# Kernel optimization log

Measured on AMD Instinct MI355X. Metric: run time of the kernel, lower is better.

## Reference

```python
import jax, jax.numpy as jnp
import numpy as np

NDIV = (10, 10)
OUT_CHANNEL = 100


def setup_inputs() -> dict:
    key = jax.random.key(0)
    k1, k2 = jax.random.split(key)
    x1 = jax.random.normal(k1, (8, 64, 128, 128), dtype=jnp.float32)
    x2 = jax.random.normal(k2, (8, 64, 60, 60), dtype=jnp.float32)
    return {"x1": x1, "x2": x2}


def reference(x1, x2):
    B, C, H, W = x1.shape
    h, w = x2.shape[-2], x2.shape[-1]
    nd0, nd1 = NDIV
    hh, ww = h // nd0, w // nd1  # patch size (6, 6)
    P = nd0 * nd1                # 100 patches per sample

    # channel-wise L2 normalization (dim=1)
    x1n = x1 / jnp.linalg.norm(x1, axis=1, keepdims=True)
    x2n = x2 / jnp.linalg.norm(x2, axis=1, keepdims=True)

    # extract nd0*nd1 patches per sample as conv filters: [B*P, C, hh, ww]
    patches = x2n.reshape(B, C, nd0, hh, nd1, ww)
    patches = patches.transpose(0, 2, 4, 1, 3, 5).reshape(B * P, C, hh, ww)

    # grouped cross-correlation (torch F.conv2d = correlation, no kernel flip)
    lhs = x1n.reshape(1, B * C, H, W)
    mm = jax.lax.conv_general_dilated(
        lhs, patches,
        window_strides=(1, 1),
        padding=((hh // 2, hh // 2), (ww // 2, ww // 2)),
        feature_group_count=B,
        dimension_numbers=("NCHW", "OIHW", "NCHW"),
    ) / (hh * ww)  # [1, B*P, H+1, W+1] for even hh,ww

    # bilinear resize to (H, W)  (torch align_corners=False == half-pixel)
    mm = jax.image.resize(mm, (1, B * P, H, W), method="bilinear")

    # [B, P, H, W] -> topk over patch dim, then mean
    mm = mm.reshape(B, P, H, W)
    topv = jax.lax.top_k(jnp.moveaxis(mm, 1, -1), OUT_CHANNEL)[0]  # [B,H,W,k]
    out = jnp.mean(topv, axis=-1)[:, None]  # [B,1,H,W]
    return out
```

## Files before the change

kernel.cpp:

```cpp
#include <hip/hip_runtime.h>
#include <cstddef>
#include <cstdint>

#define BB   8
#define CC   64
#define H1   128
#define W1   128
#define HW1  (H1*W1)
#define HS   60
#define WS   60
#define HO   129
#define WO   129
#define NPIX (HS*WS)

#define UPL  (BB*HW1)

typedef _Float16 f16;
typedef __attribute__((ext_vector_type(2))) _Float16 h2;

#if __has_builtin(__builtin_amdgcn_fdot2)
#define FDOT2(a, b, c) __builtin_amdgcn_fdot2((a), (b), (c), false)
#else
#define FDOT2(a, b, c) ((c) + (float)(a)[0] * (float)(b)[0] + (float)(a)[1] * (float)(b)[1])
#endif

static __device__ __forceinline__ h2 pack_h2(float lo, float hi) {
#if __has_builtin(__builtin_amdgcn_cvt_pkrtz)
    return __builtin_bit_cast(h2, __builtin_amdgcn_cvt_pkrtz(lo, hi));
#else
    h2 r; r[0] = (f16)lo; r[1] = (f16)hi; return r;
#endif
}

__global__ __launch_bounds__(256) void k_inv2(const float* __restrict__ x2,
                                              float* __restrict__ inv2) {
    __shared__ float red[256];
    int tid = threadIdx.x;
    int pix = blockIdx.x * 64 + (tid & 63);
    int q   = tid >> 6;

    int b  = pix / NPIX;
    int hw = pix - b * NPIX;
    const float* p = x2 + (size_t)b * CC * NPIX + (size_t)(q * 16) * NPIX + hw;

    float s = 0.f;
#pragma unroll
    for (int cc = 0; cc < 16; cc += 8) {
        float v0 = p[(cc+0)*NPIX], v1 = p[(cc+1)*NPIX];
        float v2 = p[(cc+2)*NPIX], v3 = p[(cc+3)*NPIX];
        float v4 = p[(cc+4)*NPIX], v5 = p[(cc+5)*NPIX];
        float v6 = p[(cc+6)*NPIX], v7 = p[(cc+7)*NPIX];
        s += v0*v0 + v1*v1 + v2*v2 + v3*v3 + v4*v4 + v5*v5 + v6*v6 + v7*v7;
    }
    red[tid] = s;
    __syncthreads();
    if (tid < 64) {
        float t = red[tid] + red[tid + 64] + red[tid + 128] + red[tid + 192];
        inv2[blockIdx.x * 64 + tid] = 1.0f / sqrtf(t);
    }
}

__global__ __launch_bounds__(256) void k_fold(const float* __restrict__ x2,
                                              const float* __restrict__ inv2,
                                              f16* __restrict__ Sh) {
    __shared__ __align__(16) float pl[NPIX];
    __shared__ float red[256];
    int tid = threadIdx.x;
    int bc  = blockIdx.x;
    int b   = bc >> 6;
    int c   = bc & 63;

    const float* px = x2 + (size_t)bc * NPIX;
    const float* pn = inv2 + (size_t)b * NPIX;

    const float4* px4 = (const float4*)px;
    const float4* pn4 = (const float4*)pn;
    float4* pl4 = (float4*)pl;
    for (int i = tid; i < NPIX / 4; i += 256) {
        float4 a = px4[i];
        float4 w = pn4[i];
        pl4[i] = make_float4(a.x * w.x, a.y * w.y, a.z * w.z, a.w * w.w);
    }
    __syncthreads();

    float s = 0.f;
    if (tid < 252) {
        int bin = tid / 7, k = tid - bin * 7;
        int r = bin / 6, c6 = bin - r * 6;
        for (int e = k; e < 100; e += 7) {
            int i = e / 10, j = e - i * 10;
            s += pl[(r + 6 * i) * WS + (c6 + 6 * j)];
        }
    }
    red[tid] = s;
    __syncthreads();

    if (tid < 36) {
        const float* q = red + tid * 7;
        float bin = q[0] + q[1] + q[2] + q[3] + q[4] + q[5] + q[6];
        Sh[(((size_t)b * 32 + (c >> 1)) * 36 + tid) * 2 + (c & 1)] = (f16)bin;
    }
}

__global__ __launch_bounds__(256) void k_gemm(const float* __restrict__ x1,
                                              const f16* __restrict__ Sh,
                                              f16* __restrict__ U) {
    int blk = (blockIdx.x & 7) * 64 + (blockIdx.x >> 3);
    int b = blk >> 6;
    int p = (blk & 63) * 256 + threadIdx.x;

    const float* xp = x1 + (size_t)b * CC * HW1 + p;
    const uint32_t* Sw = (const uint32_t*)Sh + (size_t)b * (32 * 36);

    float acc[36];
#pragma unroll
    for (int t = 0; t < 36; ++t) acc[t] = 0.f;
    float s2 = 0.f;

#pragma unroll 2
    for (int cc = 0; cc < CC; cc += 8) {
        float v[8];
#pragma unroll
        for (int j = 0; j < 8; ++j)
            v[j] = __builtin_nontemporal_load(&xp[(size_t)(cc + j) * HW1]);
        h2 a[4];
#pragma unroll
        for (int q = 0; q < 4; ++q) {
            a[q] = pack_h2(v[2*q], v[2*q+1]);
            s2 += v[2*q] * v[2*q] + v[2*q+1] * v[2*q+1];
        }
#pragma unroll
        for (int q = 0; q < 4; ++q) {
            const uint32_t* sq = Sw + (size_t)(cc / 2 + q) * 36;
#pragma unroll
            for (int t = 0; t < 36; ++t) {
                h2 sv = __builtin_bit_cast(h2, sq[t]);
                acc[t] = FDOT2(a[q], sv, acc[t]);
            }
        }
    }

    float inv = (1.0f / 3600.0f) / sqrtf(s2);
    f16* up = U + (size_t)b * HW1 + p;
#pragma unroll
    for (int t = 0; t < 36; ++t) up[(size_t)t * UPL] = (f16)(acc[t] * inv);
}

__global__ __launch_bounds__(256) void k_out(const f16* __restrict__ U,
                                             float* __restrict__ out) {
    __shared__ float m[20 * 21];
    int blk  = (blockIdx.x & 7) * 64 + (blockIdx.x >> 3);
    int b    = blk >> 6;
    int tile = blk & 63;
    int oy0 = (tile >> 3) * 16, ox0 = (tile & 7) * 16;
    int ry0 = oy0 - 1, rx0 = ox0 - 1;
    int tid = threadIdx.x;

    const f16* Ub = U + (size_t)b * HW1;

    bool interior = (ry0 >= 3) && (ry0 + 19 <= 125) && (rx0 >= 3) && (rx0 + 19 <= 125);

    if (interior) {
        const f16* base = Ub + (size_t)(ry0 - 3) * W1 + (rx0 - 3);
        for (int i = tid; i < 400; i += 256) {
            int ly = i / 20, lx = i - ly * 20;
            const f16* pp = base + (size_t)ly * W1 + lx;
            float s = 0.f;
#pragma unroll
            for (int t = 0; t < 36; ++t) {
                int dy = t / 6, dx = t - dy * 6;
                s += (float)pp[(size_t)t * UPL + dy * W1 + dx];
            }
            m[ly * 21 + lx] = s;
        }
    } else {
        for (int i = tid; i < 400; i += 256) {
            int ly = i / 20, lx = i - ly * 20;
            int jy = min(max(ry0 + ly, 0), 128);
            int jx = min(max(rx0 + lx, 0), 128);
            float s = 0.f;
#pragma unroll
            for (int t = 0; t < 36; ++t) {
                int dy = t / 6, dx = t - dy * 6;
                int py = jy - 3 + dy, px = jx - 3 + dx;
                if ((unsigned)py < 128u && (unsigned)px < 128u)
                    s += (float)Ub[(size_t)t * UPL + py * W1 + px];
            }
            m[ly * 21 + lx] = s;
        }
    }
    __syncthreads();

    const float inv_scale = 129.0f / 128.0f;
    const float ksc       = 128.0f / 129.0f;

    int oy = oy0 + (tid >> 4);
    int ox = ox0 + (tid & 15);

    float sy = (oy + 0.5f) * inv_scale - 0.5f;
    float sx = (ox + 0.5f) * inv_scale - 0.5f;
    int fy = (int)floorf(sy);
    int fx = (int)floorf(sx);

    float wy[4], wx[4];
    float sumy = 0.f, sumx = 0.f;
#pragma unroll
    for (int k = 0; k < 4; ++k) {
        int jy = fy - 1 + k;
        float w = 0.f;
        if (jy >= 0 && jy < HO) w = fmaxf(0.f, 1.0f - fabsf(sy - (float)jy) * ksc);
        wy[k] = w; sumy += w;
        int jx = fx - 1 + k;
        float w2 = 0.f;
        if (jx >= 0 && jx < WO) w2 = fmaxf(0.f, 1.0f - fabsf(sx - (float)jx) * ksc);
        wx[k] = w2; sumx += w2;
    }

    float r = 0.f;
#pragma unroll
    for (int ky = 0; ky < 4; ++ky) {
        if (wy[ky] == 0.f) continue;
        int ly = fy - 1 + ky - ry0;
        float rowv = 0.f;
#pragma unroll
        for (int kx = 0; kx < 4; ++kx) {
            if (wx[kx] == 0.f) continue;
            int lx = fx - 1 + kx - rx0;
            rowv += wx[kx] * m[ly * 21 + lx];
        }
        r += wy[ky] * rowv;
    }

    out[(size_t)b * HW1 + oy * W1 + ox] = r / (sumy * sumx);
}

extern "C" void kernel_launch(void* const* d_in, const int* in_sizes, int n_in,
                              void* d_out, int out_size, void* d_ws, size_t ws_size,
                              hipStream_t stream) {
    const float* x1 = (const float*)d_in[0];
    const float* x2 = (const float*)d_in[1];
    float* out = (float*)d_out;

    float* ws   = (float*)d_ws;
    float* inv2 = ws;
    f16*   Sh   = (f16*)(inv2 + BB * NPIX);
    f16*   U    = (f16*)((char*)Sh + (size_t)BB * CC * 36 * sizeof(f16));

    k_inv2<<<BB * NPIX / 64, 256, 0, stream>>>(x2, inv2);
    k_fold<<<BB * CC, 256, 0, stream>>>(x2, inv2, Sh);
    k_gemm<<<BB * 64, 256, 0, stream>>>(x1, Sh, U);
    k_out <<<BB * 64, 256, 0, stream>>>(U, out);
}
```

Baseline: 114.5 us.

## Fuse four stage kernels into one cooperative kernel with grid syncs

Merges the inv-norm, fold, GEMM and resize/output kernels into a single persistent cooperative kernel, with grid-wide barriers between stages. This removes three kernel launch boundaries and their drain/ramp gaps. In exchange it adds grid.sync overhead and a launch-bounds occupancy hint that may constrain registers for the 36-accumulator GEMM stage. It also relies on all 512 blocks being co-resident for the cooperative launch to succeed.

```diff
diff --git a/kernel.cpp b/kernel.cpp
--- a/kernel.cpp
+++ b/kernel.cpp
@@ -1,6 +1,9 @@
 #include <hip/hip_runtime.h>
+#include <hip/hip_cooperative_groups.h>
 #include <cstddef>
 #include <cstdint>
+
+namespace cg = cooperative_groups;
 
 #define BB   8
 #define CC   64
@@ -32,206 +35,208 @@
 #endif
 }
 
-__global__ __launch_bounds__(256) void k_inv2(const float* __restrict__ x2,
-                                              float* __restrict__ inv2) {
-    __shared__ float red[256];
+__global__ __launch_bounds__(256, 2) void k_all(const float* __restrict__ x1,
+                                                const float* __restrict__ x2,
+                                                float* __restrict__ inv2,
+                                                f16* __restrict__ Sh,
+                                                f16* __restrict__ U,
+                                                float* __restrict__ out) {
+    cg::grid_group grid = cg::this_grid();
+    __shared__ __align__(16) float smem[NPIX + 256];
+
     int tid = threadIdx.x;
-    int pix = blockIdx.x * 64 + (tid & 63);
-    int q   = tid >> 6;
-
-    int b  = pix / NPIX;
-    int hw = pix - b * NPIX;
-    const float* p = x2 + (size_t)b * CC * NPIX + (size_t)(q * 16) * NPIX + hw;
-
-    float s = 0.f;
-#pragma unroll
-    for (int cc = 0; cc < 16; cc += 8) {
-        float v0 = p[(cc+0)*NPIX], v1 = p[(cc+1)*NPIX];
-        float v2 = p[(cc+2)*NPIX], v3 = p[(cc+3)*NPIX];
-        float v4 = p[(cc+4)*NPIX], v5 = p[(cc+5)*NPIX];
-        float v6 = p[(cc+6)*NPIX], v7 = p[(cc+7)*NPIX];
-        s += v0*v0 + v1*v1 + v2*v2 + v3*v3 + v4*v4 + v5*v5 + v6*v6 + v7*v7;
-    }
-    red[tid] = s;
-    __syncthreads();
-    if (tid < 64) {
-        float t = red[tid] + red[tid + 64] + red[tid + 128] + red[tid + 192];
-        inv2[blockIdx.x * 64 + tid] = 1.0f / sqrtf(t);
-    }
-}
-
-__global__ __launch_bounds__(256) void k_fold(const float* __restrict__ x2,
-                                              const float* __restrict__ inv2,
-                                              f16* __restrict__ Sh) {
-    __shared__ __align__(16) float pl[NPIX];
-    __shared__ float red[256];
-    int tid = threadIdx.x;
-    int bc  = blockIdx.x;
-    int b   = bc >> 6;
-    int c   = bc & 63;
-
-    const float* px = x2 + (size_t)bc * NPIX;
-    const float* pn = inv2 + (size_t)b * NPIX;
-
-    const float4* px4 = (const float4*)px;
-    const float4* pn4 = (const float4*)pn;
-    float4* pl4 = (float4*)pl;
-    for (int i = tid; i < NPIX / 4; i += 256) {
-        float4 a = px4[i];
-        float4 w = pn4[i];
-        pl4[i] = make_float4(a.x * w.x, a.y * w.y, a.z * w.z, a.w * w.w);
-    }
-    __syncthreads();
-
-    float s = 0.f;
-    if (tid < 252) {
-        int bin = tid / 7, k = tid - bin * 7;
-        int r = bin / 6, c6 = bin - r * 6;
-        for (int e = k; e < 100; e += 7) {
-            int i = e / 10, j = e - i * 10;
-            s += pl[(r + 6 * i) * WS + (c6 + 6 * j)];
-        }
-    }
-    red[tid] = s;
-    __syncthreads();
-
-    if (tid < 36) {
-        const float* q = red + tid * 7;
-        float bin = q[0] + q[1] + q[2] + q[3] + q[4] + q[5] + q[6];
-        Sh[(((size_t)b * 32 + (c >> 1)) * 36 + tid) * 2 + (c & 1)] = (f16)bin;
-    }
-}
-
-__global__ __launch_bounds__(256) void k_gemm(const float* __restrict__ x1,
-                                              const f16* __restrict__ Sh,
-                                              f16* __restrict__ U) {
-    int blk = (blockIdx.x & 7) * 64 + (blockIdx.x >> 3);
-    int b = blk >> 6;
-    int p = (blk & 63) * 256 + threadIdx.x;
-
-    const float* xp = x1 + (size_t)b * CC * HW1 + p;
-    const uint32_t* Sw = (const uint32_t*)Sh + (size_t)b * (32 * 36);
-
-    float acc[36];
-#pragma unroll
-    for (int t = 0; t < 36; ++t) acc[t] = 0.f;
-    float s2 = 0.f;
+    int blk0 = blockIdx.x;
+
+    if (blk0 < 450) {
+        float* red = smem;
+        int pix = blk0 * 64 + (tid & 63);
+        int q   = tid >> 6;
+        int b  = pix / NPIX;
+        int hw = pix - b * NPIX;
+        const float* p = x2 + (size_t)b * CC * NPIX + (size_t)(q * 16) * NPIX + hw;
+        float s = 0.f;
+#pragma unroll
+        for (int cc = 0; cc < 16; cc += 8) {
+            float v0 = p[(cc+0)*NPIX], v1 = p[(cc+1)*NPIX];
+            float v2 = p[(cc+2)*NPIX], v3 = p[(cc+3)*NPIX];
+            float v4 = p[(cc+4)*NPIX], v5 = p[(cc+5)*NPIX];
+            float v6 = p[(cc+6)*NPIX], v7 = p[(cc+7)*NPIX];
+            s += v0*v0 + v1*v1 + v2*v2 + v3*v3 + v4*v4 + v5*v5 + v6*v6 + v7*v7;
+        }
+        red[tid] = s;
+        __syncthreads();
+        if (tid < 64) {
+            float t = red[tid] + red[tid + 64] + red[tid + 128] + red[tid + 192];
+            inv2[blk0 * 64 + tid] = 1.0f / sqrtf(t);
+        }
+    }
+    grid.sync();
+
+    {
+        float* pl  = smem;
+        float* red = smem + NPIX;
+        int bc = blk0;
+        int b  = bc >> 6;
+        int c  = bc & 63;
+
+        const float4* px4 = (const float4*)(x2 + (size_t)bc * NPIX);
+        const float4* pn4 = (const float4*)(inv2 + (size_t)b * NPIX);
+        float4* pl4 = (float4*)pl;
+        for (int i = tid; i < NPIX / 4; i += 256) {
+            float4 a = px4[i];
+            float4 w = pn4[i];
+            pl4[i] = make_float4(a.x * w.x, a.y * w.y, a.z * w.z, a.w * w.w);
+        }
+        __syncthreads();
+
+        float s = 0.f;
+        if (tid < 252) {
+            int bin = tid / 7, k = tid - bin * 7;
+            int r = bin / 6, c6 = bin - r * 6;
+            for (int e = k; e < 100; e += 7) {
+                int i = e / 10, j = e - i * 10;
+                s += pl[(r + 6 * i) * WS + (c6 + 6 * j)];
+            }
+        }
+        red[tid] = s;
+        __syncthreads();
+
+        if (tid < 36) {
+            const float* q = red + tid * 7;
+            float bin = q[0] + q[1] + q[2] + q[3] + q[4] + q[5] + q[6];
+            Sh[(((size_t)b * 32 + (c >> 1)) * 36 + tid) * 2 + (c & 1)] = (f16)bin;
+        }
+    }
+    grid.sync();
+
+    {
+        int blk = (blk0 & 7) * 64 + (blk0 >> 3);
+        int b = blk >> 6;
+        int p = (blk & 63) * 256 + tid;
+
+        const float* xp = x1 + (size_t)b * CC * HW1 + p;
+        const uint32_t* Sw = (const uint32_t*)Sh + (size_t)b * (32 * 36);
+
+        float acc[36];
+#pragma unroll
+        for (int t = 0; t < 36; ++t) acc[t] = 0.f;
+        float s2 = 0.f;
 
 #pragma unroll 2
-    for (int cc = 0; cc < CC; cc += 8) {
-        float v[8];
-#pragma unroll
-        for (int j = 0; j < 8; ++j)
-            v[j] = __builtin_nontemporal_load(&xp[(size_t)(cc + j) * HW1]);
-        h2 a[4];
-#pragma unroll
-        for (int q = 0; q < 4; ++q) {
-            a[q] = pack_h2(v[2*q], v[2*q+1]);
-            s2 += v[2*q] * v[2*q] + v[2*q+1] * v[2*q+1];
-        }
-#pragma unroll
-        for (int q = 0; q < 4; ++q) {
-            const uint32_t* sq = Sw + (size_t)(cc / 2 + q) * 36;
-#pragma unroll
-            for (int t = 0; t < 36; ++t) {
-                h2 sv = __builtin_bit_cast(h2, sq[t]);
-                acc[t] = FDOT2(a[q], sv, acc[t]);
-            }
-        }
-    }
-
-    float inv = (1.0f / 3600.0f) / sqrtf(s2);
-    f16* up = U + (size_t)b * HW1 + p;
-#pragma unroll
-    for (int t = 0; t < 36; ++t) up[(size_t)t * UPL] = (f16)(acc[t] * inv);
-}
-
-__global__ __launch_bounds__(256) void k_out(const f16* __restrict__ U,
-                                             float* __restrict__ out) {
-    __shared__ float m[20 * 21];
-    int blk  = (blockIdx.x & 7) * 64 + (blockIdx.x >> 3);
-    int b    = blk >> 6;
-    int tile = blk & 63;
-    int oy0 = (tile >> 3) * 16, ox0 = (tile & 7) * 16;
-    int ry0 = oy0 - 1, rx0 = ox0 - 1;
-    int tid = threadIdx.x;
-
-    const f16* Ub = U + (size_t)b * HW1;
-
-    bool interior = (ry0 >= 3) && (ry0 + 19 <= 125) && (rx0 >= 3) && (rx0 + 19 <= 125);
-
-    if (interior) {
-        const f16* base = Ub + (size_t)(ry0 - 3) * W1 + (rx0 - 3);
-        for (int i = tid; i < 400; i += 256) {
-            int ly = i / 20, lx = i - ly * 20;
-            const f16* pp = base + (size_t)ly * W1 + lx;
-            float s = 0.f;
-#pragma unroll
-            for (int t = 0; t < 36; ++t) {
-                int dy = t / 6, dx = t - dy * 6;
-                s += (float)pp[(size_t)t * UPL + dy * W1 + dx];
-            }
-            m[ly * 21 + lx] = s;
-        }
-    } else {
-        for (int i = tid; i < 400; i += 256) {
-            int ly = i / 20, lx = i - ly * 20;
-            int jy = min(max(ry0 + ly, 0), 128);
-            int jx = min(max(rx0 + lx, 0), 128);
-            float s = 0.f;
-#pragma unroll
-            for (int t = 0; t < 36; ++t) {
-                int dy = t / 6, dx = t - dy * 6;
-                int py = jy - 3 + dy, px = jx - 3 + dx;
-                if ((unsigned)py < 128u && (unsigned)px < 128u)
-                    s += (float)Ub[(size_t)t * UPL + py * W1 + px];
-            }
-            m[ly * 21 + lx] = s;
-        }
-    }
-    __syncthreads();
-
-    const float inv_scale = 129.0f / 128.0f;
-    const float ksc       = 128.0f / 129.0f;
-
-    int oy = oy0 + (tid >> 4);
-    int ox = ox0 + (tid & 15);
-
-    float sy = (oy + 0.5f) * inv_scale - 0.5f;
-    float sx = (ox + 0.5f) * inv_scale - 0.5f;
-    int fy = (int)floorf(sy);
-    int fx = (int)floorf(sx);
-
-    float wy[4], wx[4];
-    float sumy = 0.f, sumx = 0.f;
-#pragma unroll
-    for (int k = 0; k < 4; ++k) {
-        int jy = fy - 1 + k;
-        float w = 0.f;
-        if (jy >= 0 && jy < HO) w = fmaxf(0.f, 1.0f - fabsf(sy - (float)jy) * ksc);
-        wy[k] = w; sumy += w;
-        int jx = fx - 1 + k;
-        float w2 = 0.f;
-        if (jx >= 0 && jx < WO) w2 = fmaxf(0.f, 1.0f - fabsf(sx - (float)jx) * ksc);
-        wx[k] = w2; sumx += w2;
-    }
-
-    float r = 0.f;
-#pragma unroll
-    for (int ky = 0; ky < 4; ++ky) {
-        if (wy[ky] == 0.f) continue;
-        int ly = fy - 1 + ky - ry0;
-        float rowv = 0.f;
-#pragma unroll
-        for (int kx = 0; kx < 4; ++kx) {
-            if (wx[kx] == 0.f) continue;
-            int lx = fx - 1 + kx - rx0;
-            rowv += wx[kx] * m[ly * 21 + lx];
-        }
-        r += wy[ky] * rowv;
-    }
-
-    out[(size_t)b * HW1 + oy * W1 + ox] = r / (sumy * sumx);
+        for (int cc = 0; cc < CC; cc += 8) {
+            float v[8];
+#pragma unroll
+            for (int j = 0; j < 8; ++j)
+                v[j] = __builtin_nontemporal_load(&xp[(size_t)(cc + j) * HW1]);
+            h2 a[4];
+#pragma unroll
+            for (int q = 0; q < 4; ++q) {
+                a[q] = pack_h2(v[2*q], v[2*q+1]);
+                s2 += v[2*q] * v[2*q] + v[2*q+1] * v[2*q+1];
+            }
+#pragma unroll
+            for (int q = 0; q < 4; ++q) {
+                const uint32_t* sq = Sw + (size_t)(cc / 2 + q) * 36;
+#pragma unroll
+                for (int t = 0; t < 36; ++t) {
+                    h2 sv = __builtin_bit_cast(h2, sq[t]);
+                    acc[t] = FDOT2(a[q], sv, acc[t]);
+                }
+            }
+        }
+
+        float inv = (1.0f / 3600.0f) / sqrtf(s2);
+        f16* up = U + (size_t)b * HW1 + p;
+#pragma unroll
+        for (int t = 0; t < 36; ++t) up[(size_t)t * UPL] = (f16)(acc[t] * inv);
+    }
+    grid.sync();
+
+    {
+        float* m = smem;
+        int blk  = (blk0 & 7) * 64 + (blk0 >> 3);
+        int b    = blk >> 6;
+        int tile = blk & 63;
+        int oy0 = (tile >> 3) * 16, ox0 = (tile & 7) * 16;
+        int ry0 = oy0 - 1, rx0 = ox0 - 1;
+
+        const f16* Ub = U + (size_t)b * HW1;
+
+        bool interior = (ry0 >= 3) && (ry0 + 19 <= 125) && (rx0 >= 3) && (rx0 + 19 <= 125);
+
+        if (interior) {
+            const f16* base = Ub + (size_t)(ry0 - 3) * W1 + (rx0 - 3);
+            for (int i = tid; i < 400; i += 256) {
+                int ly = i / 20, lx = i - ly * 20;
+                const f16* pp = base + (size_t)ly * W1 + lx;
+                float s = 0.f;
+#pragma unroll
+                for (int t = 0; t < 36; ++t) {
+                    int dy = t / 6, dx = t - dy * 6;
+                    s += (float)pp[(size_t)t * UPL + dy * W1 + dx];
+                }
+                m[ly * 21 + lx] = s;
+            }
+        } else {
+            for (int i = tid; i < 400; i += 256) {
+                int ly = i / 20, lx = i - ly * 20;
+                int jy = min(max(ry0 + ly, 0), 128);
+                int jx = min(max(rx0 + lx, 0), 128);
+                float s = 0.f;
+#pragma unroll
+                for (int t = 0; t < 36; ++t) {
+                    int dy = t / 6, dx = t - dy * 6;
+                    int py = jy - 3 + dy, px = jx - 3 + dx;
+                    if ((unsigned)py < 128u && (unsigned)px < 128u)
+                        s += (float)Ub[(size_t)t * UPL + py * W1 + px];
+                }
+                m[ly * 21 + lx] = s;
+            }
+        }
+        __syncthreads();
+
+        const float inv_scale = 129.0f / 128.0f;
+        const float ksc       = 128.0f / 129.0f;
+
+        int oy = oy0 + (tid >> 4);
+        int ox = ox0 + (tid & 15);
+
+        float sy = (oy + 0.5f) * inv_scale - 0.5f;
+        float sx = (ox + 0.5f) * inv_scale - 0.5f;
+        int fy = (int)floorf(sy);
+        int fx = (int)floorf(sx);
+
+        float wy[4], wx[4];
+        float sumy = 0.f, sumx = 0.f;
+#pragma unroll
+        for (int k = 0; k < 4; ++k) {
+            int jy = fy - 1 + k;
+            float w = 0.f;
+            if (jy >= 0 && jy < HO) w = fmaxf(0.f, 1.0f - fabsf(sy - (float)jy) * ksc);
+            wy[k] = w; sumy += w;
+            int jx = fx - 1 + k;
+            float w2 = 0.f;
+            if (jx >= 0 && jx < WO) w2 = fmaxf(0.f, 1.0f - fabsf(sx - (float)jx) * ksc);
+            wx[k] = w2; sumx += w2;
+        }
+
+        float r = 0.f;
+#pragma unroll
+        for (int ky = 0; ky < 4; ++ky) {
+            if (wy[ky] == 0.f) continue;
+            int ly = fy - 1 + ky - ry0;
+            float rowv = 0.f;
+#pragma unroll
+            for (int kx = 0; kx < 4; ++kx) {
+                if (wx[kx] == 0.f) continue;
+                int lx = fx - 1 + kx - rx0;
+                rowv += wx[kx] * m[ly * 21 + lx];
+            }
+            r += wy[ky] * rowv;
+        }
+
+        out[(size_t)b * HW1 + oy * W1 + ox] = r / (sumy * sumx);
+    }
 }
 
 extern "C" void kernel_launch(void* const* d_in, const int* in_sizes, int n_in,
@@ -246,8 +251,8 @@
     f16*   Sh   = (f16*)(inv2 + BB * NPIX);
     f16*   U    = (f16*)((char*)Sh + (size_t)BB * CC * 36 * sizeof(f16));
 
-    k_inv2<<<BB * NPIX / 64, 256, 0, stream>>>(x2, inv2);
-    k_fold<<<BB * CC, 256, 0, stream>>>(x2, inv2, Sh);
-    k_gemm<<<BB * 64, 256, 0, stream>>>(x1, Sh, U);
-    k_out <<<BB * 64, 256, 0, stream>>>(U, out);
+    void* args[] = {(void*)&x1, (void*)&x2, (void*)&inv2, (void*)&Sh,
+                    (void*)&U, (void*)&out};
+    hipLaunchCooperativeKernel(reinterpret_cast<void*>(k_all),
+                               dim3(BB * 64), dim3(256), args, 0, stream);
 }
```

After: 322.0 us. +181.3%, slower.
